# Optimization experiments

Measured on AMD Instinct MI355X. Metric: run time of the kernel, lower is better.

Reference implementation:

```python
import jax, jax.numpy as jnp
import numpy as np

B, L = 16, 4096
D_IN, D_OUT, D_MODEL, N_LAYERS, N_STATE = 257, 257, 256, 4, 32  # 32 complex modes (= d_state 64 real)


def setup_inputs() -> dict:
    key = jax.random.key(0)
    ks = iter(jax.random.split(key, 24))
    nrm = lambda shape, s=0.02: jax.random.normal(next(ks), shape, jnp.float32) * s
    H, N = D_MODEL, N_STATE
    return {
        "x": jax.random.normal(next(ks), (B, L, D_IN, 2), jnp.float32),
        "enc_Wr": nrm((D_MODEL, D_IN)), "enc_Wi": nrm((D_MODEL, D_IN)),
        "enc_br": jnp.zeros((D_MODEL,), jnp.float32), "enc_bi": jnp.zeros((D_MODEL,), jnp.float32),
        # per layer (N_LAYERS) and per complex branch (2: real-branch S4D, imag-branch S4D)
        "s4_log_dt": jax.random.uniform(next(ks), (N_LAYERS, 2, H), jnp.float32,
                                        minval=float(np.log(0.001)), maxval=float(np.log(0.1))),
        "s4_log_A_real": jnp.broadcast_to(jnp.log(0.5 * jnp.ones((H, N), jnp.float32)), (N_LAYERS, 2, H, N)) + 0.0,
        "s4_A_imag": jnp.broadcast_to(jnp.pi * jnp.arange(N, dtype=jnp.float32), (N_LAYERS, 2, H, N)) + 0.0,
        "s4_C": jax.random.normal(next(ks), (N_LAYERS, 2, H, N, 2), jnp.float32) * (0.5 ** 0.5),
        "s4_D": jax.random.normal(next(ks), (N_LAYERS, 2, H), jnp.float32),
        "s4_Wout": nrm((N_LAYERS, 2, 2 * H, H)), "s4_bout": jnp.zeros((N_LAYERS, 2, 2 * H), jnp.float32),
        "ln_gamma": jnp.ones((N_LAYERS, 2, H), jnp.float32), "ln_beta": jnp.zeros((N_LAYERS, 2, H), jnp.float32),
        "dec_Wr": nrm((D_OUT, D_MODEL)), "dec_Wi": nrm((D_OUT, D_MODEL)),
        "dec_br": jnp.zeros((D_OUT,), jnp.float32), "dec_bi": jnp.zeros((D_OUT,), jnp.float32),
    }


def complex_linear(xr, xi, Wr, Wi, br, bi):
    yr = xr @ Wr.T - xi @ Wi.T + br
    yi = xr @ Wi.T + xi @ Wr.T + bi
    return yr, yi


def s4d_branch(u, log_dt, log_A_real, A_imag, C2, D, Wout, bout):
    """Standard S4D-minimal layer. u: (B, H, L) real."""
    Ln = u.shape[-1]
    dt = jnp.exp(log_dt)                            # (H,)
    A = -jnp.exp(log_A_real) + 1j * A_imag          # (H, N) complex
    C = C2[..., 0] + 1j * C2[..., 1]                # (H, N)
    dtA = A * dt[:, None]                           # (H, N)
    Cmod = C * (jnp.exp(dtA) - 1.0) / A
    vand = jnp.exp(dtA[..., None] * jnp.arange(Ln)) # (H, N, L)
    k = 2.0 * jnp.einsum('hn,hnl->hl', Cmod, vand).real  # (H, L)
    kf = jnp.fft.rfft(k, n=2 * Ln)
    uf = jnp.fft.rfft(u, n=2 * Ln)
    y = jnp.fft.irfft(uf * kf[None], n=2 * Ln)[..., :Ln]  # causal conv
    y = y + u * D[:, None]
    y = jax.nn.gelu(y, approximate=False)
    y = jnp.einsum('oh,bhl->bol', Wout, y) + bout[None, :, None]  # 1x1 conv to 2H
    a, g = jnp.split(y, 2, axis=1)                  # GLU over channel dim
    return a * jax.nn.sigmoid(g)


def layer_norm(x, gamma, beta):
    # x: (B, L, H), normalize over H (biased variance, like torch LayerNorm)
    mu = x.mean(-1, keepdims=True)
    var = x.var(-1, keepdims=True)
    return (x - mu) / jnp.sqrt(var + 1e-5) * gamma + beta


def reference(x, enc_Wr, enc_Wi, enc_br, enc_bi,
              s4_log_dt, s4_log_A_real, s4_A_imag, s4_C, s4_D, s4_Wout, s4_bout,
              ln_gamma, ln_beta, dec_Wr, dec_Wi, dec_br, dec_bi):
    xr, xi = complex_linear(x[..., 0], x[..., 1], enc_Wr, enc_Wi, enc_br, enc_bi)  # (B, L, H)
    xr = xr.swapaxes(-1, -2)  # (B, H, L)
    xi = xi.swapaxes(-1, -2)
    for l in range(N_LAYERS):
        sr = lambda u: s4d_branch(u, s4_log_dt[l, 0], s4_log_A_real[l, 0], s4_A_imag[l, 0],
                                  s4_C[l, 0], s4_D[l, 0], s4_Wout[l, 0], s4_bout[l, 0])
        si = lambda u: s4d_branch(u, s4_log_dt[l, 1], s4_log_A_real[l, 1], s4_A_imag[l, 1],
                                  s4_C[l, 1], s4_D[l, 1], s4_Wout[l, 1], s4_bout[l, 1])
        zr = sr(xr) - si(xi)
        zi = sr(xi) + si(xr)
        xr = xr + zr  # residual (dropout = identity)
        xi = xi + zi
        # post-norm over d_model (separate LN for real/imag parts)
        xr = layer_norm(xr.swapaxes(-1, -2), ln_gamma[l, 0], ln_beta[l, 0]).swapaxes(-1, -2)
        xi = layer_norm(xi.swapaxes(-1, -2), ln_gamma[l, 1], ln_beta[l, 1]).swapaxes(-1, -2)
    xr = xr.swapaxes(-1, -2)  # (B, L, H)
    xi = xi.swapaxes(-1, -2)
    yr, yi = complex_linear(xr, xi, dec_Wr, dec_Wi, dec_br, dec_bi)  # (B, L, D_OUT)
    return jnp.stack([yr, yi], axis=-1)
```

## Files before the change

### kernel.cpp

```cpp
#include <hip/hip_runtime.h>

typedef unsigned short ushort_t;
typedef unsigned int uint_t;
typedef __attribute__((ext_vector_type(8))) short short8;
typedef __attribute__((ext_vector_type(4))) float f32x4;

#define B_    16
#define L_    4096
#define H_    256
#define N_    32
#define DIN_  257
#define DOUT_ 257
#define NL_   4
#define Q_    128
#define NC_   32
#define BL_   (B_*L_)
#define NH_   (N_*H_)
#define PLANE_ 16777216
#define SSZ_  4194304

__device__ __forceinline__ float bfu(ushort_t u) {
    union { uint_t i; float f; } v; v.i = ((uint_t)u) << 16; return v.f;
}
__device__ __forceinline__ ushort_t f2bf(float f) {
    union { float f; uint_t i; } v; v.f = f;
    uint_t x = v.i;
    return (ushort_t)((x + 0x7FFFu + ((x >> 16) & 1u)) >> 16);
}
__device__ __forceinline__ uint2 pack4(float a, float b, float c, float d) {
    uint2 r;
    r.x = (uint_t)f2bf(a) | ((uint_t)f2bf(b) << 16);
    r.y = (uint_t)f2bf(c) | ((uint_t)f2bf(d) << 16);
    return r;
}
__device__ __forceinline__ float ldi(const void* p, size_t i, int f32) {
    return f32 ? ((const float*)p)[i] : bfu(((const ushort_t*)p)[i]);
}

__device__ __forceinline__ void gl16(const ushort_t* g, ushort_t* l) {
    __builtin_amdgcn_global_load_lds(
        (const __attribute__((address_space(1))) uint_t*)g,
        (__attribute__((address_space(3))) uint_t*)l, 16, 0, 0);
}

__device__ __forceinline__ uint4 ld8bf(const void* W, size_t eoff, int f32) {
    uint4 r;
    if (f32) {
        const float* p = (const float*)W + eoff;
        float4 a = *(const float4*)p;
        float4 b = *(const float4*)(p + 4);
        r.x = (uint_t)f2bf(a.x) | ((uint_t)f2bf(a.y) << 16);
        r.y = (uint_t)f2bf(a.z) | ((uint_t)f2bf(a.w) << 16);
        r.z = (uint_t)f2bf(b.x) | ((uint_t)f2bf(b.y) << 16);
        r.w = (uint_t)f2bf(b.z) | ((uint_t)f2bf(b.w) << 16);
    } else {
        r = *(const uint4*)((const ushort_t*)W + eoff);
    }
    return r;
}

__device__ __forceinline__ short8 negbf(short8 v) {
    short8 r;
#pragma unroll
    for (int i = 0; i < 8; ++i) r[i] = (short)(v[i] ^ (short)0x8000);
    return r;
}

#define MFMA16(a, b, c) __builtin_amdgcn_mfma_f32_16x16x32_bf16((a), (b), (c), 0, 0, 0)

__global__ void probe_kernel(const void* __restrict__ x, int* __restrict__ flag) {
    __shared__ int cnt;
    if (threadIdx.x == 0) cnt = 0;
    __syncthreads();
    uint_t w = ((const uint_t*)x)[threadIdx.x];
    float f = bfu((ushort_t)(w & 0xFFFF));
    float a = fabsf(f);
    if (a > 1e-5f && a < 100.f) atomicAdd(&cnt, 1);
    __syncthreads();
    if (threadIdx.x == 0) *flag = (cnt > 128) ? 0 : 1;
}

__global__ __launch_bounds__(256) void param_kernel(
        const void* __restrict__ log_dt, const void* __restrict__ lAr,
        const void* __restrict__ Aim, const void* __restrict__ C2,
        float* __restrict__ params, const int* __restrict__ dfl) {
    int f32 = *dfl;
    int idx = blockIdx.x * 256 + threadIdx.x;
    int h  = idx & (H_ - 1);
    int n  = (idx >> 8) & (N_ - 1);
    int lb = idx >> 13;
    float dt = expf(ldi(log_dt, lb * H_ + h, f32));
    size_t pin = (size_t)(lb * H_ + h) * N_ + n;
    float Ar = -expf(ldi(lAr, pin, f32));
    float Ai = ldi(Aim, pin, f32);
    float Cr = ldi(C2, pin * 2, f32), Ci = ldi(C2, pin * 2 + 1, f32);
    float dr = Ar * dt, di = Ai * dt;
    float e  = expf(dr);
    float wr = e * cosf(di), wi = e * sinf(di);
    float Er = wr - 1.0f, Ei = wi;
    float inv = 1.0f / (Ar * Ar + Ai * Ai);
    float Fr = (Er * Ar + Ei * Ai) * inv;
    float Fi = (Ei * Ar - Er * Ai) * inv;
    float ctr = 2.0f * (Cr * Fr - Ci * Fi);
    float cti = 2.0f * (Cr * Fi + Ci * Fr);
    float eq = expf((float)Q_ * dr);
    float ph = (float)Q_ * di;
    float wqr = eq * cosf(ph), wqi = eq * sinf(ph);
    float* pb = params + (size_t)lb * 6 * NH_;
    int o = n * H_ + h;
    pb[0 * NH_ + o] = wr;  pb[1 * NH_ + o] = wi;
    pb[2 * NH_ + o] = ctr; pb[3 * NH_ + o] = cti;
    pb[4 * NH_ + o] = wqr; pb[5 * NH_ + o] = wqi;
}

__global__ __launch_bounds__(256) void repack_x(
        const void* __restrict__ x, ushort_t* __restrict__ xre,
        ushort_t* __restrict__ xim, const int* __restrict__ dfl) {
    int f32 = *dfl;
    size_t i = ((size_t)blockIdx.x * 256 + threadIdx.x) * 4;
    int row = (int)(i >> 8);
    int k = (int)(i & 255);
    size_t src = (size_t)row * DIN_ + k;
    float re[4], im[4];
#pragma unroll
    for (int j = 0; j < 4; ++j) {
        if (f32) {
            float2 v = ((const float2*)x)[src + j];
            re[j] = v.x; im[j] = v.y;
        } else {
            uint_t v = ((const uint_t*)x)[src + j];
            re[j] = bfu((ushort_t)(v & 0xFFFF));
            im[j] = bfu((ushort_t)(v >> 16));
        }
    }
    *(uint2*)(xre + i) = pack4(re[0], re[1], re[2], re[3]);
    *(uint2*)(xim + i) = pack4(im[0], im[1], im[2], im[3]);
}

__global__ __launch_bounds__(256) void pack_encw(
        const void* __restrict__ Wr, const void* __restrict__ Wi,
        ushort_t* __restrict__ Wpr, ushort_t* __restrict__ Wpi,
        const int* __restrict__ dfl) {
    int f32 = *dfl;
    int n = blockIdx.x, k = threadIdx.x;
    Wpr[n * 256 + k] = f2bf(ldi(Wr, (size_t)n * DIN_ + k, f32));
    Wpi[n * 256 + k] = f2bf(ldi(Wi, (size_t)n * DIN_ + k, f32));
}

__global__ __launch_bounds__(256) void enc_gemm(
        const ushort_t* __restrict__ xre, const ushort_t* __restrict__ xim,
        const ushort_t* __restrict__ Wpr, const ushort_t* __restrict__ Wpi,
        const void* __restrict__ x, const void* __restrict__ eWr,
        const void* __restrict__ eWi, const void* __restrict__ br,
        const void* __restrict__ bi, ushort_t* __restrict__ xr,
        ushort_t* __restrict__ xi_, const int* __restrict__ dfl) {
    __shared__ __align__(16) ushort_t Ars[8192];
    __shared__ __align__(16) ushort_t Ais[8192];
    __shared__ __align__(16) ushort_t Brs[4096];
    __shared__ __align__(16) ushort_t Bis[4096];
    int f32 = *dfl;
    int m0 = blockIdx.x * 128, n0 = blockIdx.y * 64;
    int tid = threadIdx.x;
    int w = tid >> 6, l = tid & 63;
    int rb = w * 32;
    int lr = l & 15, lk = (l >> 4) << 4, lsw = (l & 7) << 4;
    int arow = tid >> 3;
    int acb  = ((tid & 7) << 4) ^ ((arow & 7) << 4);
    int brow = tid >> 2;
    int bq   = (tid & 3) << 5;
    int bsw  = (brow & 7) << 4;
    int wrow = n0 + brow;
    f32x4 z4 = {0.f, 0.f, 0.f, 0.f};
    f32x4 aR[2][4], aI[2][4];
#pragma unroll
    for (int mi = 0; mi < 2; ++mi)
#pragma unroll
        for (int nj = 0; nj < 4; ++nj) { aR[mi][nj] = z4; aI[mi][nj] = z4; }

    for (int k0 = 0; k0 < H_; k0 += 64) {
        if (k0) __syncthreads();
        {
            size_t so = (size_t)(m0 + arow) * H_ + k0 + (acb >> 1);
            ushort_t* dr = Ars + tid * 8;
            ushort_t* di = Ais + tid * 8;
#pragma unroll
            for (int ch = 0; ch < 4; ++ch) {
                gl16(xre + so + (size_t)ch * 32 * H_, dr + ch * 2048);
                gl16(xim + so + (size_t)ch * 32 * H_, di + ch * 2048);
            }
        }
        {
            char* pr_ = (char*)Brs + brow * 128;
            char* pi_ = (char*)Bis + brow * 128;
#pragma unroll
            for (int cc = 0; cc < 2; ++cc) {
                int cb = bq + cc * 16;
                *(uint4*)(pr_ + (cb ^ bsw)) =
                    *(const uint4*)(Wpr + (size_t)wrow * H_ + k0 + (cb >> 1));
                *(uint4*)(pi_ + (cb ^ bsw)) =
                    *(const uint4*)(Wpi + (size_t)wrow * H_ + k0 + (cb >> 1));
            }
        }
        __syncthreads();
#pragma unroll
        for (int ks = 0; ks < 2; ++ks) {
            int off = (ks * 64 + lk) ^ lsw;
            short8 x0 = *(const short8*)((const char*)Ars + (rb + lr) * 128 + off);
            short8 x1 = *(const short8*)((const char*)Ars + (rb + 16 + lr) * 128 + off);
            short8 y0 = *(const short8*)((const char*)Ais + (rb + lr) * 128 + off);
            short8 y1 = *(const short8*)((const char*)Ais + (rb + 16 + lr) * 128 + off);
#pragma unroll
            for (int nj = 0; nj < 4; ++nj) {
                short8 wr_ = *(const short8*)((const char*)Brs + (nj * 16 + lr) * 128 + off);
                short8 wi_ = *(const short8*)((const char*)Bis + (nj * 16 + lr) * 128 + off);
                short8 wn = negbf(wi_);
                aR[0][nj] = MFMA16(x0, wr_, aR[0][nj]);
                aR[0][nj] = MFMA16(y0, wn,  aR[0][nj]);
                aR[1][nj] = MFMA16(x1, wr_, aR[1][nj]);
                aR[1][nj] = MFMA16(y1, wn,  aR[1][nj]);
                aI[0][nj] = MFMA16(x0, wi_, aI[0][nj]);
                aI[0][nj] = MFMA16(y0, wr_, aI[0][nj]);
                aI[1][nj] = MFMA16(x1, wi_, aI[1][nj]);
                aI[1][nj] = MFMA16(y1, wr_, aI[1][nj]);
            }
        }
    }
    float xcr[8], xci[8];
#pragma unroll
    for (int mi = 0; mi < 2; ++mi)
#pragma unroll
        for (int r = 0; r < 4; ++r) {
            int row = m0 + rb + mi * 16 + ((l >> 4) << 2) + r;
            size_t pi = (size_t)row * DIN_ + 256;
            float re, im;
            if (f32) { float2 v = ((const float2*)x)[pi]; re = v.x; im = v.y; }
            else { uint_t v = ((const uint_t*)x)[pi];
                   re = bfu((ushort_t)(v & 0xFFFF)); im = bfu((ushort_t)(v >> 16)); }
            xcr[mi * 4 + r] = re; xci[mi * 4 + r] = im;
        }
#pragma unroll
    for (int nj = 0; nj < 4; ++nj) {
        int col = n0 + nj * 16 + lr;
        float wcr = ldi(eWr, (size_t)col * DIN_ + 256, f32);
        float wci = ldi(eWi, (size_t)col * DIN_ + 256, f32);
        float bR = ldi(br, col, f32), bI = ldi(bi, col, f32);
#pragma unroll
        for (int mi = 0; mi < 2; ++mi)
#pragma unroll
            for (int r = 0; r < 4; ++r) {
                int row = m0 + rb + mi * 16 + ((l >> 4) << 2) + r;
                int q = mi * 4 + r;
                float re = aR[mi][nj][r] + xcr[q] * wcr - xci[q] * wci + bR;
                float im = aI[mi][nj][r] + xcr[q] * wci + xci[q] * wcr + bI;
                size_t off = (size_t)row * H_ + col;
                xr[off]  = f2bf(re);
                xi_[off] = f2bf(im);
            }
    }
}

__global__ __launch_bounds__(256) void pass_a(
        const ushort_t* __restrict__ U, const float* __restrict__ P, ushort_t* __restrict__ S) {
    __shared__ __align__(16) ushort_t Us[Q_ * 64];
    int c = blockIdx.x, b = blockIdx.y, z = blockIdx.z;
    int tid = threadIdx.x;
    int hl = tid >> 2, h = z * 64 + hl;
    int nb = (tid & 3) * 8;
    const ushort_t* ub = U + (size_t)(b * L_ + c * Q_) * H_ + z * 64;
#pragma unroll
    for (int p = 0; p < 4; ++p)
        gl16(ub + (size_t)(p * 32 + (tid >> 3)) * H_ + (tid & 7) * 8,
             Us + p * 2048 + tid * 8);
    float wr[8], wi[8], sr[8], si[8];
#pragma unroll
    for (int n = 0; n < 8; ++n) {
        wr[n] = P[(nb + n) * H_ + h]; wi[n] = P[NH_ + (nb + n) * H_ + h];
        sr[n] = 0.f; si[n] = 0.f;
    }
    __syncthreads();
    float uvn = bfu(Us[hl]);
    for (int t = 0; t < Q_; ++t) {
        float uv = uvn;
        int tn = (t + 1 < Q_) ? t + 1 : t;
        uvn = bfu(Us[tn * 64 + hl]);
#pragma unroll
        for (int n = 0; n < 8; ++n) {
            float nr = fmaf(wr[n], sr[n], fmaf(-wi[n], si[n], uv));
            si[n] = fmaf(wr[n], si[n], wi[n] * sr[n]);
            sr[n] = nr;
        }
    }
    size_t o = (size_t)(b * NC_ + c) * N_ * H_ + h;
#pragma unroll
    for (int n = 0; n < 8; ++n) {
        S[o + (nb + n) * H_] = f2bf(sr[n]);
        S[o + (nb + n) * H_ + SSZ_] = f2bf(si[n]);
    }
}

__global__ __launch_bounds__(256) void pass_b(
        const float* __restrict__ P, ushort_t* __restrict__ S) {
    int n = blockIdx.x, b = blockIdx.y, h = threadIdx.x;
    float wqr = P[4 * NH_ + n * H_ + h], wqi = P[5 * NH_ + n * H_ + h];
    float Xr = 0.f, Xi = 0.f;
    size_t idx = ((size_t)(b * NC_) * N_ + n) * H_ + h;
    float nlr = bfu(S[idx]), nli = bfu(S[idx + SSZ_]);
    for (int c = 0; c < NC_; ++c) {
        float lr = nlr, li = nli;
        if (c + 1 < NC_) {
            nlr = bfu(S[idx + NH_]);
            nli = bfu(S[idx + NH_ + SSZ_]);
        }
        S[idx] = f2bf(Xr); S[idx + SSZ_] = f2bf(Xi);
        float nr = fmaf(wqr, Xr, fmaf(-wqi, Xi, lr));
        Xi = fmaf(wqr, Xi, fmaf(wqi, Xr, li));
        Xr = nr;
        idx += NH_;
    }
}

__global__ __launch_bounds__(256) void pass_c(
        const ushort_t* __restrict__ U, const float* __restrict__ P,
        const ushort_t* __restrict__ S, const void* __restrict__ Dp, int doff,
        ushort_t* __restrict__ G, const int* __restrict__ dfl) {
    __shared__ __align__(16) ushort_t Us[Q_ * 64];
    int f32 = *dfl;
    int c = blockIdx.x, b = blockIdx.y, z = blockIdx.z;
    int tid = threadIdx.x;
    int hl = tid >> 2, h = z * 64 + hl;
    int nb = (tid & 3) * 8;
    const ushort_t* ub = U + (size_t)(b * L_ + c * Q_) * H_ + z * 64;
#pragma unroll
    for (int p = 0; p < 4; ++p)
        gl16(ub + (size_t)(p * 32 + (tid >> 3)) * H_ + (tid & 7) * 8,
             Us + p * 2048 + tid * 8);
    float wr[8], wi[8], cr[8], ci[8], sr[8], si[8];
#pragma unroll
    for (int i = 0; i < 8; ++i) {
        int o = (nb + i) * H_ + h;
        wr[i] = P[o]; wi[i] = P[NH_ + o];
        cr[i] = P[2 * NH_ + o]; ci[i] = P[3 * NH_ + o];
    }
    size_t so = (size_t)(b * NC_ + c) * N_ * H_ + h;
#pragma unroll
    for (int i = 0; i < 8; ++i) {
        sr[i] = bfu(S[so + (nb + i) * H_]);
        si[i] = bfu(S[so + (nb + i) * H_ + SSZ_]);
    }
    float Dv = ldi(Dp, (size_t)doff + h, f32);
    ushort_t* g = G + (size_t)(b * L_ + c * Q_) * H_ + h;
    __syncthreads();
    float uvn = bfu(Us[hl]);
    for (int t = 0; t < Q_; ++t) {
        float uv = uvn;
        int tn = (t + 1 < Q_) ? t + 1 : t;
        uvn = bfu(Us[tn * 64 + hl]);
        float a0 = 0.f, a1 = 0.f;
#pragma unroll
        for (int i = 0; i < 8; ++i) {
            float nr = fmaf(wr[i], sr[i], fmaf(-wi[i], si[i], uv));
            si[i] = fmaf(wr[i], si[i], wi[i] * sr[i]);
            sr[i] = nr;
            if (i & 1) a1 = fmaf(cr[i], sr[i], fmaf(-ci[i], si[i], a1));
            else       a0 = fmaf(cr[i], sr[i], fmaf(-ci[i], si[i], a0));
        }
        float acc = a0 + a1;
        acc += __shfl_xor(acc, 1, 64);
        acc += __shfl_xor(acc, 2, 64);
        float y = fmaf(Dv, uv, acc);
        float ge = 0.5f * y * (1.0f + erff(y * 0.70710678118654752f));
        if ((tid & 3) == 0) g[(size_t)t * H_] = f2bf(ge);
    }
}

__global__ __launch_bounds__(256) void wout_gemm(
        const ushort_t* __restrict__ Gb, const void* __restrict__ W, size_t woff,
        const void* __restrict__ bo, int boff, ushort_t* __restrict__ Z, int mode,
        const int* __restrict__ dfl) {
    __shared__ __align__(16) ushort_t As[8192];
    __shared__ __align__(16) ushort_t Bs[8192];
    int f32 = *dfl;
    int m0 = blockIdx.x * 128, n0 = blockIdx.y * 64;
    int tid = threadIdx.x;
    int w = tid >> 6, l = tid & 63;
    int rb = w * 32;
    int lr = l & 15, lk = (l >> 4) << 4;
    int lsw = (l & 7) << 4;
    int arow = tid >> 3;
    int acb  = ((tid & 7) << 4) ^ ((arow & 7) << 4);
    int brow = tid >> 1;
    int bhalf = (tid & 1) << 6;
    int bsw = (brow & 7) << 4;
    int wrow = (brow < 64) ? (n0 + brow) : (192 + n0 + brow);
    f32x4 z4 = {0.f, 0.f, 0.f, 0.f};
    f32x4 acc[2][8];
#pragma unroll
    for (int mi = 0; mi < 2; ++mi)
#pragma unroll
        for (int nj = 0; nj < 8; ++nj) acc[mi][nj] = z4;

    for (int k0 = 0; k0 < H_; k0 += 64) {
        if (k0) __syncthreads();
        {
            const ushort_t* src = Gb + (size_t)(m0 + arow) * H_ + k0 + (acb >> 1);
            ushort_t* dst = As + tid * 8;
#pragma unroll
            for (int ch = 0; ch < 4; ++ch)
                gl16(src + (size_t)ch * 32 * H_, dst + ch * 2048);
        }
        {
            size_t wb = woff + (size_t)wrow * H_ + k0;
            char* bp = (char*)Bs + brow * 128;
#pragma unroll
            for (int cc = 0; cc < 4; ++cc) {
                int cb = bhalf + cc * 16;
                uint4 v = ld8bf(W, wb + (cb >> 1), f32);
                *(uint4*)(bp + (cb ^ bsw)) = v;
            }
        }
        __syncthreads();
#pragma unroll
        for (int ks = 0; ks < 2; ++ks) {
            int off = (ks * 64 + lk) ^ lsw;
            short8 a0 = *(const short8*)((const char*)As + (rb + lr) * 128 + off);
            short8 a1 = *(const short8*)((const char*)As + (rb + 16 + lr) * 128 + off);
#pragma unroll
            for (int nj = 0; nj < 8; ++nj) {
                short8 bv = *(const short8*)((const char*)Bs + (nj * 16 + lr) * 128 + off);
                acc[0][nj] = MFMA16(a0, bv, acc[0][nj]);
                acc[1][nj] = MFMA16(a1, bv, acc[1][nj]);
            }
        }
    }
    float ba[4], bg[4];
#pragma unroll
    for (int nj = 0; nj < 4; ++nj) {
        ba[nj] = ldi(bo, (size_t)boff + n0 + nj * 16 + lr, f32);
        bg[nj] = ldi(bo, (size_t)boff + 256 + n0 + nj * 16 + lr, f32);
    }
#pragma unroll
    for (int mi = 0; mi < 2; ++mi)
#pragma unroll
        for (int nj = 0; nj < 4; ++nj)
#pragma unroll
            for (int r = 0; r < 4; ++r) {
                float av = acc[mi][nj][r] + ba[nj];
                float gv = acc[mi][nj + 4][r] + bg[nj];
                float s = av * (1.0f / (1.0f + expf(-gv)));
                int row = m0 + rb + mi * 16 + ((l >> 4) << 2) + r;
                size_t zo = (size_t)row * H_ + n0 + nj * 16 + lr;
                if (mode == 0)      Z[zo] = f2bf(s);
                else if (mode == 1) Z[zo] = f2bf(bfu(Z[zo]) + s);
                else                Z[zo] = f2bf(bfu(Z[zo]) - s);
            }
}

__global__ __launch_bounds__(256) void combine_ln(
        ushort_t* __restrict__ xr, ushort_t* __restrict__ xi,
        const ushort_t* __restrict__ zr, const ushort_t* __restrict__ zi,
        const void* __restrict__ gamma, const void* __restrict__ beta, int layer,
        const int* __restrict__ dfl) {
    int f32 = *dfl;
    int tid = threadIdx.x;
    int wv = tid >> 6, l = tid & 63;
    size_t row = (size_t)blockIdx.x * 4 + wv;
    size_t base = row * H_ + l * 4;
    uint2 vr2 = *(const uint2*)(xr + base);
    uint2 vi2 = *(const uint2*)(xi + base);
    uint2 zr2 = *(const uint2*)(zr + base);
    uint2 zi2 = *(const uint2*)(zi + base);
    float vr[4], vi[4];
    vr[0] = bfu((ushort_t)(vr2.x & 0xFFFF)) + bfu((ushort_t)(zr2.x & 0xFFFF));
    vr[1] = bfu((ushort_t)(vr2.x >> 16))    + bfu((ushort_t)(zr2.x >> 16));
    vr[2] = bfu((ushort_t)(vr2.y & 0xFFFF)) + bfu((ushort_t)(zr2.y & 0xFFFF));
    vr[3] = bfu((ushort_t)(vr2.y >> 16))    + bfu((ushort_t)(zr2.y >> 16));
    vi[0] = bfu((ushort_t)(vi2.x & 0xFFFF)) + bfu((ushort_t)(zi2.x & 0xFFFF));
    vi[1] = bfu((ushort_t)(vi2.x >> 16))    + bfu((ushort_t)(zi2.x >> 16));
    vi[2] = bfu((ushort_t)(vi2.y & 0xFFFF)) + bfu((ushort_t)(zi2.y & 0xFFFF));
    vi[3] = bfu((ushort_t)(vi2.y >> 16))    + bfu((ushort_t)(zi2.y >> 16));
    float s0 = 0.f, s1 = 0.f, s2 = 0.f, s3 = 0.f;
#pragma unroll
    for (int j = 0; j < 4; ++j) {
        s0 += vr[j]; s1 += vr[j] * vr[j];
        s2 += vi[j]; s3 += vi[j] * vi[j];
    }
#pragma unroll
    for (int off = 32; off >= 1; off >>= 1) {
        s0 += __shfl_xor(s0, off, 64); s1 += __shfl_xor(s1, off, 64);
        s2 += __shfl_xor(s2, off, 64); s3 += __shfl_xor(s3, off, 64);
    }
    const float invH = 1.0f / 256.0f;
    float mur = s0 * invH, varr = s1 * invH - mur * mur;
    float mui = s2 * invH, vari = s3 * invH - mui * mui;
    float rsr = rsqrtf(varr + 1e-5f), rsi = rsqrtf(vari + 1e-5f);
    float orv[4], oiv[4];
#pragma unroll
    for (int j = 0; j < 4; ++j) {
        int hh = l * 4 + j;
        float gr  = ldi(gamma, (size_t)(layer * 2 + 0) * H_ + hh, f32);
        float br_ = ldi(beta,  (size_t)(layer * 2 + 0) * H_ + hh, f32);
        float gi  = ldi(gamma, (size_t)(layer * 2 + 1) * H_ + hh, f32);
        float bi_ = ldi(beta,  (size_t)(layer * 2 + 1) * H_ + hh, f32);
        orv[j] = (vr[j] - mur) * rsr * gr + br_;
        oiv[j] = (vi[j] - mui) * rsi * gi + bi_;
    }
    *(uint2*)(xr + base) = pack4(orv[0], orv[1], orv[2], orv[3]);
    *(uint2*)(xi + base) = pack4(oiv[0], oiv[1], oiv[2], oiv[3]);
}

__global__ __launch_bounds__(256) void dec_gemm(
        const ushort_t* __restrict__ xr, const ushort_t* __restrict__ xi,
        const void* __restrict__ Wr, const void* __restrict__ Wi,
        const void* __restrict__ br, const void* __restrict__ bi,
        void* __restrict__ out, const int* __restrict__ dfl) {
    __shared__ __align__(16) ushort_t Ars[8192];
    __shared__ __align__(16) ushort_t Ais[8192];
    __shared__ __align__(16) ushort_t Brs[4096];
    __shared__ __align__(16) ushort_t Bis[4096];
    int f32 = *dfl;
    int m0 = blockIdx.x * 128, n0 = blockIdx.y * 64;
    int tid = threadIdx.x;
    int w = tid >> 6, l = tid & 63;
    int rb = w * 32;
    int lr = l & 15, lk = (l >> 4) << 4, lsw = (l & 7) << 4;
    int arow = tid >> 3;
    int acb  = ((tid & 7) << 4) ^ ((arow & 7) << 4);
    int brow = tid >> 2;
    int bq   = (tid & 3) << 5;
    int bsw  = (brow & 7) << 4;
    int wrow = n0 + brow;
    bool bvalid = wrow < DOUT_;
    uint4 zz; zz.x = zz.y = zz.z = zz.w = 0u;
    f32x4 z4 = {0.f, 0.f, 0.f, 0.f};
    f32x4 aR[2][4], aI[2][4];
#pragma unroll
    for (int mi = 0; mi < 2; ++mi)
#pragma unroll
        for (int nj = 0; nj < 4; ++nj) { aR[mi][nj] = z4; aI[mi][nj] = z4; }

    for (int k0 = 0; k0 < H_; k0 += 64) {
        if (k0) __syncthreads();
        {
            size_t so = (size_t)(m0 + arow) * H_ + k0 + (acb >> 1);
            ushort_t* dr = Ars + tid * 8;
            ushort_t* di = Ais + tid * 8;
#pragma unroll
            for (int ch = 0; ch < 4; ++ch) {
                gl16(xr + so + (size_t)ch * 32 * H_, dr + ch * 2048);
                gl16(xi + so + (size_t)ch * 32 * H_, di + ch * 2048);
            }
        }
        {
            size_t wb = (size_t)wrow * H_ + k0 + (bq >> 1);
            char* pr_ = (char*)Brs + brow * 128;
            char* pi_ = (char*)Bis + brow * 128;
#pragma unroll
            for (int cc = 0; cc < 2; ++cc) {
                int cb = bq + cc * 16;
                uint4 vr = zz, vi = zz;
                if (bvalid) {
                    vr = ld8bf(Wr, wb + cc * 8, f32);
                    vi = ld8bf(Wi, wb + cc * 8, f32);
                }
                *(uint4*)(pr_ + (cb ^ bsw)) = vr;
                *(uint4*)(pi_ + (cb ^ bsw)) = vi;
            }
        }
        __syncthreads();
#pragma unroll
        for (int ks = 0; ks < 2; ++ks) {
            int off = (ks * 64 + lk) ^ lsw;
            short8 x0 = *(const short8*)((const char*)Ars + (rb + lr) * 128 + off);
            short8 x1 = *(const short8*)((const char*)Ars + (rb + 16 + lr) * 128 + off);
            short8 y0 = *(const short8*)((const char*)Ais + (rb + lr) * 128 + off);
            short8 y1 = *(const short8*)((const char*)Ais + (rb + 16 + lr) * 128 + off);
#pragma unroll
            for (int nj = 0; nj < 4; ++nj) {
                short8 wr_ = *(const short8*)((const char*)Brs + (nj * 16 + lr) * 128 + off);
                short8 wi_ = *(const short8*)((const char*)Bis + (nj * 16 + lr) * 128 + off);
                short8 wn = negbf(wi_);
                aR[0][nj] = MFMA16(x0, wr_, aR[0][nj]);
                aR[0][nj] = MFMA16(y0, wn,  aR[0][nj]);
                aR[1][nj] = MFMA16(x1, wr_, aR[1][nj]);
                aR[1][nj] = MFMA16(y1, wn,  aR[1][nj]);
                aI[0][nj] = MFMA16(x0, wi_, aI[0][nj]);
                aI[0][nj] = MFMA16(y0, wr_, aI[0][nj]);
                aI[1][nj] = MFMA16(x1, wi_, aI[1][nj]);
                aI[1][nj] = MFMA16(y1, wr_, aI[1][nj]);
            }
        }
    }
#pragma unroll
    for (int nj = 0; nj < 4; ++nj) {
        int col = n0 + nj * 16 + lr;
        if (col < DOUT_) {
            float bR = ldi(br, col, f32), bI = ldi(bi, col, f32);
#pragma unroll
            for (int mi = 0; mi < 2; ++mi)
#pragma unroll
                for (int r = 0; r < 4; ++r) {
                    int row = m0 + rb + mi * 16 + ((l >> 4) << 2) + r;
                    size_t pi = (size_t)row * DOUT_ + col;
                    float re = aR[mi][nj][r] + bR;
                    float im = aI[mi][nj][r] + bI;
                    if (f32) {
                        ((float2*)out)[pi] = make_float2(re, im);
                    } else {
                        ((uint_t*)out)[pi] = (uint_t)f2bf(re) | ((uint_t)f2bf(im) << 16);
                    }
                }
        }
    }
}

extern "C" void kernel_launch(void* const* d_in, const int* in_sizes, int n_in,
                              void* d_out, int out_size, void* d_ws, size_t ws_size,
                              hipStream_t stream) {
    const void* x      = d_in[0];
    const void* enc_Wr = d_in[1];
    const void* enc_Wi = d_in[2];
    const void* enc_br = d_in[3];
    const void* enc_bi = d_in[4];
    const void* log_dt = d_in[5];
    const void* lAr    = d_in[6];
    const void* Aim    = d_in[7];
    const void* C2     = d_in[8];
    const void* Dp     = d_in[9];
    const void* Wout   = d_in[10];
    const void* bout   = d_in[11];
    const void* gamma  = d_in[12];
    const void* beta   = d_in[13];
    const void* dec_Wr = d_in[14];
    const void* dec_Wi = d_in[15];
    const void* dec_br = d_in[16];
    const void* dec_bi = d_in[17];

    ushort_t* xr = (ushort_t*)d_ws;
    ushort_t* xi = xr + (size_t)PLANE_;
    ushort_t* gb = xi + (size_t)PLANE_;
    ushort_t* st = gb + (size_t)PLANE_;
    int*      fl = (int*)(st + (size_t)2 * SSZ_);
    float*    pr = (float*)(fl + 64);
    ushort_t* zr = (ushort_t*)d_out;
    ushort_t* zi = zr + (size_t)PLANE_;
    ushort_t* xre = zr;
    ushort_t* xim = zi;
    ushort_t* Wpr = st;
    ushort_t* Wpi = st + 65536;

    probe_kernel<<<1, 256, 0, stream>>>(x, fl);
    param_kernel<<<256, 256, 0, stream>>>(log_dt, lAr, Aim, C2, pr, fl);
    repack_x<<<16384, 256, 0, stream>>>(x, xre, xim, fl);
    pack_encw<<<256, 256, 0, stream>>>(enc_Wr, enc_Wi, Wpr, Wpi, fl);
    enc_gemm<<<dim3(BL_ / 128, H_ / 64), 256, 0, stream>>>(xre, xim, Wpr, Wpi,
            x, enc_Wr, enc_Wi, enc_br, enc_bi, xr, xi, fl);

    for (int l = 0; l < NL_; ++l) {
        struct App { int br; const ushort_t* U; ushort_t* Zt; int mode; };
        App apps[4] = {
            {0, xr, zr, 0},
            {1, xi, zr, 2},
            {0, xi, zi, 0},
            {1, xr, zi, 1},
        };
        for (int a = 0; a < 4; ++a) {
            const float* P = pr + (size_t)(l * 2 + apps[a].br) * 6 * NH_;
            pass_a<<<dim3(NC_, B_, 4), 256, 0, stream>>>(apps[a].U, P, st);
            pass_b<<<dim3(N_, B_), 256, 0, stream>>>(P, st);
            pass_c<<<dim3(NC_, B_, 4), 256, 0, stream>>>(apps[a].U, P, st,
                    Dp, (l * 2 + apps[a].br) * H_, gb, fl);
            wout_gemm<<<dim3(BL_ / 128, H_ / 64), 256, 0, stream>>>(gb,
                    Wout, (size_t)(l * 2 + apps[a].br) * 512 * H_,
                    bout, (l * 2 + apps[a].br) * 512,
                    apps[a].Zt, apps[a].mode, fl);
        }
        combine_ln<<<BL_ / 4, 256, 0, stream>>>(xr, xi, zr, zi, gamma, beta, l, fl);
    }

    dec_gemm<<<dim3(BL_ / 128, (DOUT_ + 63) / 64), 256, 0, stream>>>(
            xr, xi, dec_Wr, dec_Wi, dec_br, dec_bi, d_out, fl);
}
```

Before: 4.942 ms.

## Use packed float2 FMAs in chunked scan kernels with 16 modes per thread

The chunk-scan kernels pass_a and pass_c now give each thread 16 complex modes as float2 pairs instead of 8 scalar modes, so the recurrence can map to packed FMA instructions. Each block now covers 128 channels instead of 64, which halves the grid along z and shortens the cross-lane reduction to one shuffle. The LDS tile doubles. Register pressure per thread rises, which may cut occupancy, and there are half as many blocks to hide latency.

```diff
diff --git a/kernel.cpp b/kernel.cpp
--- a/kernel.cpp
+++ b/kernel.cpp
@@ -4,6 +4,7 @@
 typedef unsigned int uint_t;
 typedef __attribute__((ext_vector_type(8))) short short8;
 typedef __attribute__((ext_vector_type(4))) float f32x4;
+typedef __attribute__((ext_vector_type(2))) float f32x2;
 
 #define B_    16
 #define L_    4096
@@ -35,6 +36,14 @@
 }
 __device__ __forceinline__ float ldi(const void* p, size_t i, int f32) {
     return f32 ? ((const float*)p)[i] : bfu(((const ushort_t*)p)[i]);
+}
+
+__device__ __forceinline__ f32x2 fma2(f32x2 a, f32x2 b, f32x2 c) {
+#if __has_builtin(__builtin_elementwise_fma)
+    return __builtin_elementwise_fma(a, b, c);
+#else
+    f32x2 r; r.x = fmaf(a.x, b.x, c.x); r.y = fmaf(a.y, b.y, c.y); return r;
+#endif
 }
 
 __device__ __forceinline__ void gl16(const ushort_t* g, ushort_t* l) {
@@ -261,40 +270,50 @@
 
 __global__ __launch_bounds__(256) void pass_a(
         const ushort_t* __restrict__ U, const float* __restrict__ P, ushort_t* __restrict__ S) {
-    __shared__ __align__(16) ushort_t Us[Q_ * 64];
+    __shared__ __align__(16) ushort_t Us[Q_ * 128];
     int c = blockIdx.x, b = blockIdx.y, z = blockIdx.z;
     int tid = threadIdx.x;
-    int hl = tid >> 2, h = z * 64 + hl;
-    int nb = (tid & 3) * 8;
-    const ushort_t* ub = U + (size_t)(b * L_ + c * Q_) * H_ + z * 64;
-#pragma unroll
-    for (int p = 0; p < 4; ++p)
-        gl16(ub + (size_t)(p * 32 + (tid >> 3)) * H_ + (tid & 7) * 8,
-             Us + p * 2048 + tid * 8);
-    float wr[8], wi[8], sr[8], si[8];
-#pragma unroll
-    for (int n = 0; n < 8; ++n) {
-        wr[n] = P[(nb + n) * H_ + h]; wi[n] = P[NH_ + (nb + n) * H_ + h];
-        sr[n] = 0.f; si[n] = 0.f;
+    int wv = tid >> 6, l = tid & 63;
+    int hl = tid >> 1, h = z * 128 + hl;
+    int nb = (tid & 1) * 16;
+    const ushort_t* ub = U + (size_t)(b * L_ + c * Q_) * H_ + z * 128;
+#pragma unroll
+    for (int p = 0; p < 8; ++p) {
+        int row = p * 16 + wv * 4 + (l >> 4);
+        gl16(ub + (size_t)row * H_ + (l & 15) * 8,
+             Us + (p * 16 + wv * 4) * 128 + l * 8);
+    }
+    f32x2 wr2[8], wi2[8], sr2[8], si2[8];
+#pragma unroll
+    for (int i = 0; i < 8; ++i) {
+        int o0 = (nb + 2 * i) * H_ + h;
+        wr2[i] = f32x2{P[o0], P[o0 + H_]};
+        wi2[i] = f32x2{P[NH_ + o0], P[NH_ + o0 + H_]};
+        sr2[i] = f32x2{0.f, 0.f}; si2[i] = f32x2{0.f, 0.f};
     }
     __syncthreads();
     float uvn = bfu(Us[hl]);
     for (int t = 0; t < Q_; ++t) {
         float uv = uvn;
         int tn = (t + 1 < Q_) ? t + 1 : t;
-        uvn = bfu(Us[tn * 64 + hl]);
-#pragma unroll
-        for (int n = 0; n < 8; ++n) {
-            float nr = fmaf(wr[n], sr[n], fmaf(-wi[n], si[n], uv));
-            si[n] = fmaf(wr[n], si[n], wi[n] * sr[n]);
-            sr[n] = nr;
+        uvn = bfu(Us[tn * 128 + hl]);
+        f32x2 uvv = {uv, uv};
+#pragma unroll
+        for (int i = 0; i < 8; ++i) {
+            f32x2 t1 = fma2(-wi2[i], si2[i], uvv);
+            f32x2 nr = fma2(wr2[i], sr2[i], t1);
+            f32x2 t2 = wi2[i] * sr2[i];
+            si2[i] = fma2(wr2[i], si2[i], t2);
+            sr2[i] = nr;
         }
     }
     size_t o = (size_t)(b * NC_ + c) * N_ * H_ + h;
 #pragma unroll
-    for (int n = 0; n < 8; ++n) {
-        S[o + (nb + n) * H_] = f2bf(sr[n]);
-        S[o + (nb + n) * H_ + SSZ_] = f2bf(si[n]);
+    for (int i = 0; i < 8; ++i) {
+        S[o + (nb + 2 * i) * H_]            = f2bf(sr2[i].x);
+        S[o + (nb + 2 * i + 1) * H_]        = f2bf(sr2[i].y);
+        S[o + (nb + 2 * i) * H_ + SSZ_]     = f2bf(si2[i].x);
+        S[o + (nb + 2 * i + 1) * H_ + SSZ_] = f2bf(si2[i].y);
     }
 }
 
@@ -323,29 +342,36 @@
         const ushort_t* __restrict__ U, const float* __restrict__ P,
         const ushort_t* __restrict__ S, const void* __restrict__ Dp, int doff,
         ushort_t* __restrict__ G, const int* __restrict__ dfl) {
-    __shared__ __align__(16) ushort_t Us[Q_ * 64];
+    __shared__ __align__(16) ushort_t Us[Q_ * 128];
     int f32 = *dfl;
     int c = blockIdx.x, b = blockIdx.y, z = blockIdx.z;
     int tid = threadIdx.x;
-    int hl = tid >> 2, h = z * 64 + hl;
-    int nb = (tid & 3) * 8;
-    const ushort_t* ub = U + (size_t)(b * L_ + c * Q_) * H_ + z * 64;
-#pragma unroll
-    for (int p = 0; p < 4; ++p)
-        gl16(ub + (size_t)(p * 32 + (tid >> 3)) * H_ + (tid & 7) * 8,
-             Us + p * 2048 + tid * 8);
-    float wr[8], wi[8], cr[8], ci[8], sr[8], si[8];
+    int wv = tid >> 6, l = tid & 63;
+    int hl = tid >> 1, h = z * 128 + hl;
+    int nb = (tid & 1) * 16;
+    const ushort_t* ub = U + (size_t)(b * L_ + c * Q_) * H_ + z * 128;
+#pragma unroll
+    for (int p = 0; p < 8; ++p) {
+        int row = p * 16 + wv * 4 + (l >> 4);
+        gl16(ub + (size_t)row * H_ + (l & 15) * 8,
+             Us + (p * 16 + wv * 4) * 128 + l * 8);
+    }
+    f32x2 wr2[8], wi2[8], cr2[8], ci2[8], sr2[8], si2[8];
 #pragma unroll
     for (int i = 0; i < 8; ++i) {
-        int o = (nb + i) * H_ + h;
-        wr[i] = P[o]; wi[i] = P[NH_ + o];
-        cr[i] = P[2 * NH_ + o]; ci[i] = P[3 * NH_ + o];
+        int o0 = (nb + 2 * i) * H_ + h;
+        wr2[i] = f32x2{P[o0], P[o0 + H_]};
+        wi2[i] = f32x2{P[NH_ + o0], P[NH_ + o0 + H_]};
+        cr2[i] = f32x2{P[2 * NH_ + o0], P[2 * NH_ + o0 + H_]};
+        ci2[i] = f32x2{P[3 * NH_ + o0], P[3 * NH_ + o0 + H_]};
     }
     size_t so = (size_t)(b * NC_ + c) * N_ * H_ + h;
 #pragma unroll
     for (int i = 0; i < 8; ++i) {
-        sr[i] = bfu(S[so + (nb + i) * H_]);
-        si[i] = bfu(S[so + (nb + i) * H_ + SSZ_]);
+        sr2[i] = f32x2{bfu(S[so + (nb + 2 * i) * H_]),
+                       bfu(S[so + (nb + 2 * i + 1) * H_])};
+        si2[i] = f32x2{bfu(S[so + (nb + 2 * i) * H_ + SSZ_]),
+                       bfu(S[so + (nb + 2 * i + 1) * H_ + SSZ_])};
     }
     float Dv = ldi(Dp, (size_t)doff + h, f32);
     ushort_t* g = G + (size_t)(b * L_ + c * Q_) * H_ + h;
@@ -354,22 +380,24 @@
     for (int t = 0; t < Q_; ++t) {
         float uv = uvn;
         int tn = (t + 1 < Q_) ? t + 1 : t;
-        uvn = bfu(Us[tn * 64 + hl]);
-        float a0 = 0.f, a1 = 0.f;
+        uvn = bfu(Us[tn * 128 + hl]);
+        f32x2 uvv = {uv, uv};
+        f32x2 a2 = {0.f, 0.f};
 #pragma unroll
         for (int i = 0; i < 8; ++i) {
-            float nr = fmaf(wr[i], sr[i], fmaf(-wi[i], si[i], uv));
-            si[i] = fmaf(wr[i], si[i], wi[i] * sr[i]);
-            sr[i] = nr;
-            if (i & 1) a1 = fmaf(cr[i], sr[i], fmaf(-ci[i], si[i], a1));
-            else       a0 = fmaf(cr[i], sr[i], fmaf(-ci[i], si[i], a0));
-        }
-        float acc = a0 + a1;
+            f32x2 t1 = fma2(-wi2[i], si2[i], uvv);
+            f32x2 nr = fma2(wr2[i], sr2[i], t1);
+            f32x2 t2 = wi2[i] * sr2[i];
+            si2[i] = fma2(wr2[i], si2[i], t2);
+            sr2[i] = nr;
+            a2 = fma2(cr2[i], nr, a2);
+            a2 = fma2(-ci2[i], si2[i], a2);
+        }
+        float acc = a2.x + a2.y;
         acc += __shfl_xor(acc, 1, 64);
-        acc += __shfl_xor(acc, 2, 64);
         float y = fmaf(Dv, uv, acc);
         float ge = 0.5f * y * (1.0f + erff(y * 0.70710678118654752f));
-        if ((tid & 3) == 0) g[(size_t)t * H_] = f2bf(ge);
+        if ((tid & 1) == 0) g[(size_t)t * H_] = f2bf(ge);
     }
 }
 
@@ -665,9 +693,9 @@
         };
         for (int a = 0; a < 4; ++a) {
             const float* P = pr + (size_t)(l * 2 + apps[a].br) * 6 * NH_;
-            pass_a<<<dim3(NC_, B_, 4), 256, 0, stream>>>(apps[a].U, P, st);
+            pass_a<<<dim3(NC_, B_, 2), 256, 0, stream>>>(apps[a].U, P, st);
             pass_b<<<dim3(N_, B_), 256, 0, stream>>>(P, st);
-            pass_c<<<dim3(NC_, B_, 4), 256, 0, stream>>>(apps[a].U, P, st,
+            pass_c<<<dim3(NC_, B_, 2), 256, 0, stream>>>(apps[a].U, P, st,
                     Dp, (l * 2 + apps[a].br) * H_, gb, fl);
             wout_gemm<<<dim3(BL_ / 128, H_ / 64), 256, 0, stream>>>(gb,
                     Wout, (size_t)(l * 2 + apps[a].br) * 512 * H_,
```

Result: faster. 4.482 ms (-9.3%).
